# Kernel optimization log

Hardware: AMD Instinct MI355X
Metric: run time of the kernel (lower is better)

Reference implementation:

```python
import jax, jax.numpy as jnp
import numpy as np

C_IN = 64
C_INT = 32

def conv1x1(x, w, b):
    # x: [B,C,H,W], w: [O,C], b: [O]
    return jnp.einsum('bchw,oc->bohw', x, w) + b[None, :, None, None]

def maxpool2(x):
    # 2x2 max pool, stride 2. x: [B,C,H,W]
    B, C, H, W = x.shape
    return x.reshape(B, C, H // 2, 2, W // 2, 2).max(axis=(3, 5))

def setup_inputs() -> dict:
    key = jax.random.key(0)
    ks = jax.random.split(key, 9)
    s = 1.0 / np.sqrt(C_IN)
    si = 1.0 / np.sqrt(C_INT)
    x = jax.random.normal(ks[0], (16, C_IN, 64, 64), dtype=jnp.float32)
    return {
        'x': x,
        'w_origin': jax.random.normal(ks[1], (C_INT, C_IN), dtype=jnp.float32) * s,
        'b_origin': jax.random.normal(ks[2], (C_INT,), dtype=jnp.float32) * s,
        'w_theta': jax.random.normal(ks[3], (C_INT, C_IN), dtype=jnp.float32) * s,
        'b_theta': jax.random.normal(ks[4], (C_INT,), dtype=jnp.float32) * s,
        'w_phi': jax.random.normal(ks[5], (C_INT, C_IN), dtype=jnp.float32) * s,
        'b_phi': jax.random.normal(ks[6], (C_INT,), dtype=jnp.float32) * s,
        'w_W': jax.random.normal(ks[7], (C_IN, C_INT), dtype=jnp.float32) * si,
        'b_W': jax.random.normal(ks[8], (C_IN,), dtype=jnp.float32) * si,
    }

def reference(x, w_origin, b_origin, w_theta, b_theta, w_phi, b_phi, w_W, b_W):
    B, C, H, W = x.shape
    # value: conv1x1 + maxpool -> [B, Ci, H/2, W/2] -> [B, Nkv, Ci]
    f_x = maxpool2(conv1x1(x, w_origin, b_origin))
    f_x = f_x.reshape(B, C_INT, -1).transpose(0, 2, 1)
    # query: conv1x1 (no pooling) -> [B, N, Ci]
    theta_x = conv1x1(x, w_theta, b_theta).reshape(B, C_INT, -1).transpose(0, 2, 1)
    # key: conv1x1 + maxpool -> [B, Ci, Nkv]
    phi_x = maxpool2(conv1x1(x, w_phi, b_phi)).reshape(B, C_INT, -1)
    # attention: [B, N, Nkv]
    f = jnp.einsum('bnc,bcm->bnm', theta_x, phi_x)
    f_div_C = jax.nn.softmax(f, axis=-1)
    y = jnp.einsum('bnm,bmc->bnc', f_div_C, f_x)  # [B, N, Ci]
    y = y.transpose(0, 2, 1).reshape(B, C_INT, H, W)
    z = conv1x1(y, w_W, b_W) + x
    return z
```

## Files before the change

### kernel.cpp

```cpp
#include <hip/hip_runtime.h>
#include <math.h>


#define B_SZ 16
#define C_IN 64
#define C_INT 32
#define HW 4096
#define NKV 1024
#define PSTR 72
#define YSTR 40
#define CSTR 66
#define LOG2E 1.4426950408889634f

typedef __attribute__((ext_vector_type(8))) short bfrag;
typedef __attribute__((ext_vector_type(4))) float f32x4;

static __device__ __forceinline__ ushort f2bf(float v) {
  union { float f; uint u; } c; c.f = v;
  uint b = c.u + 0x7FFFu + ((c.u >> 16) & 1u);
  return (ushort)(b >> 16);
}
static __device__ __forceinline__ float bf2f(ushort h) {
  union { uint u; float f; } c; c.u = (uint)h << 16; return c.f;
}

__global__ __launch_bounds__(512) void k_qkv(
    const float* __restrict__ x,
    const float* __restrict__ wt, const float* __restrict__ bt,
    const float* __restrict__ wp, const float* __restrict__ bp,
    const float* __restrict__ wo, const float* __restrict__ bo,
    ushort* __restrict__ Qi, ushort* __restrict__ Ki, ushort* __restrict__ Vt) {
  __shared__ float sx[128 * CSTR];
  __shared__ float sPool[2][2][32][33];

  int t = threadIdx.x;
  int W = t >> 6, lane = t & 63, l15 = lane & 15, quad = lane >> 4;
  int bb = blockIdx.x >> 5, rg = blockIdx.x & 31;
  int p0 = rg * 128;

  #pragma unroll
  for (int i = 0; i < 4; ++i) {
    int f = i * 512 + t;
    int c = f >> 5, u = f & 31;
    float4 v = *(const float4*)(x + ((size_t)bb << 18) + (size_t)c * HW + p0 + 4 * u);
    sx[(4*u+0) * CSTR + c] = v.x;
    sx[(4*u+1) * CSTR + c] = v.y;
    sx[(4*u+2) * CSTR + c] = v.z;
    sx[(4*u+3) * CSTR + c] = v.w;
  }
  __syncthreads();

  int pix = W * 16 + l15;
  bfrag xh[2], xl[2];
  #pragma unroll
  for (int kh = 0; kh < 2; ++kh) {
    int base = pix * CSTR + kh * 32 + quad * 8;
    #pragma unroll
    for (int j2 = 0; j2 < 4; ++j2) {
      float2 d = *(const float2*)&sx[base + 2 * j2];
      ushort h0 = f2bf(d.x), h1 = f2bf(d.y);
      xh[kh][2*j2]   = (short)h0; xl[kh][2*j2]   = (short)f2bf(d.x - bf2f(h0));
      xh[kh][2*j2+1] = (short)h1; xl[kh][2*j2+1] = (short)f2bf(d.y - bf2f(h1));
    }
  }

  f32x4 acc[2];

  acc[0] = (f32x4){0.f,0.f,0.f,0.f}; acc[1] = (f32x4){0.f,0.f,0.f,0.f};
  #pragma unroll
  for (int kh = 0; kh < 2; ++kh)
    #pragma unroll
    for (int nt = 0; nt < 2; ++nt) {
      bfrag wh, wl;
      const float* wrow = wt + (size_t)(nt * 16 + l15) * 64 + kh * 32 + quad * 8;
      #pragma unroll
      for (int j = 0; j < 8; ++j) {
        float v = wrow[j] * LOG2E;
        ushort hb = f2bf(v);
        wh[j] = (short)hb; wl[j] = (short)f2bf(v - bf2f(hb));
      }
      acc[nt] = __builtin_amdgcn_mfma_f32_16x16x32_bf16(xh[kh], wh, acc[nt], 0, 0, 0);
      acc[nt] = __builtin_amdgcn_mfma_f32_16x16x32_bf16(xl[kh], wh, acc[nt], 0, 0, 0);
      acc[nt] = __builtin_amdgcn_mfma_f32_16x16x32_bf16(xh[kh], wl, acc[nt], 0, 0, 0);
    }
  #pragma unroll
  for (int nt = 0; nt < 2; ++nt) {
    float bias = bt[nt * 16 + l15] * LOG2E;
    ushort* qb = Qi + ((size_t)bb * HW + p0 + W * 16) * 64 + nt * 16 + l15;
    #pragma unroll
    for (int r = 0; r < 4; ++r) {
      float v = acc[nt][r] + bias;
      ushort hb = f2bf(v);
      qb[(size_t)(quad * 4 + r) * 64]      = hb;
      qb[(size_t)(quad * 4 + r) * 64 + 32] = f2bf(v - bf2f(hb));
    }
  }

  int prow = (W * 16 + quad * 4) >> 6;
  int px2  = ((W * 16 + quad * 4) & 63) >> 1;

  acc[0] = (f32x4){0.f,0.f,0.f,0.f}; acc[1] = (f32x4){0.f,0.f,0.f,0.f};
  #pragma unroll
  for (int kh = 0; kh < 2; ++kh)
    #pragma unroll
    for (int nt = 0; nt < 2; ++nt) {
      bfrag wh, wl;
      const float* wrow = wp + (size_t)(nt * 16 + l15) * 64 + kh * 32 + quad * 8;
      #pragma unroll
      for (int j = 0; j < 8; ++j) {
        float v = wrow[j];
        ushort hb = f2bf(v);
        wh[j] = (short)hb; wl[j] = (short)f2bf(v - bf2f(hb));
      }
      acc[nt] = __builtin_amdgcn_mfma_f32_16x16x32_bf16(xh[kh], wh, acc[nt], 0, 0, 0);
      acc[nt] = __builtin_amdgcn_mfma_f32_16x16x32_bf16(xl[kh], wh, acc[nt], 0, 0, 0);
      acc[nt] = __builtin_amdgcn_mfma_f32_16x16x32_bf16(xh[kh], wl, acc[nt], 0, 0, 0);
    }
  #pragma unroll
  for (int nt = 0; nt < 2; ++nt) {
    float bias = bp[nt * 16 + l15];
    sPool[0][prow][px2    ][nt * 16 + l15] = fmaxf(acc[nt][0], acc[nt][1]) + bias;
    sPool[0][prow][px2 + 1][nt * 16 + l15] = fmaxf(acc[nt][2], acc[nt][3]) + bias;
  }

  acc[0] = (f32x4){0.f,0.f,0.f,0.f}; acc[1] = (f32x4){0.f,0.f,0.f,0.f};
  #pragma unroll
  for (int kh = 0; kh < 2; ++kh)
    #pragma unroll
    for (int nt = 0; nt < 2; ++nt) {
      bfrag wh;
      const float* wrow = wo + (size_t)(nt * 16 + l15) * 64 + kh * 32 + quad * 8;
      #pragma unroll
      for (int j = 0; j < 8; ++j) wh[j] = (short)f2bf(wrow[j]);
      acc[nt] = __builtin_amdgcn_mfma_f32_16x16x32_bf16(xh[kh], wh, acc[nt], 0, 0, 0);
      acc[nt] = __builtin_amdgcn_mfma_f32_16x16x32_bf16(xl[kh], wh, acc[nt], 0, 0, 0);
    }
  #pragma unroll
  for (int nt = 0; nt < 2; ++nt) {
    float bias = bo[nt * 16 + l15];
    sPool[1][prow][px2    ][nt * 16 + l15] = fmaxf(acc[nt][0], acc[nt][1]) + bias;
    sPool[1][prow][px2 + 1][nt * 16 + l15] = fmaxf(acc[nt][2], acc[nt][3]) + bias;
  }
  __syncthreads();

  for (int f = t; f < 1024; f += 512) {
    int px = f >> 5, ch = f & 31;
    float v = fmaxf(sPool[0][0][px][ch], sPool[0][1][px][ch]);
    ushort hb = f2bf(v);
    size_t idx = ((size_t)bb * NKV + rg * 32 + px) * 64 + ch;
    Ki[idx] = hb;
    Ki[idx + 32] = f2bf(v - bf2f(hb));
  }
  for (int f = t; f < 1024; f += 512) {
    int ch = f >> 5, px = f & 31;
    float v = fmaxf(sPool[1][0][px][ch], sPool[1][1][px][ch]);
    Vt[(size_t)bb * 32 * NKV + (size_t)ch * NKV + rg * 32 + px] = f2bf(v);
  }
}

__global__ __launch_bounds__(256, 3) void k_attn(
    const ushort* __restrict__ Qi, const ushort* __restrict__ Ki,
    const ushort* __restrict__ Vt,
    const float* __restrict__ x, const float* __restrict__ wW,
    const float* __restrict__ bW, float* __restrict__ z) {
  __shared__ __align__(16) ushort sP[4 * 64 * PSTR];
  __shared__ __align__(16) ushort sY[2 * 64 * YSTR];

  int t = threadIdx.x;
  int w = t >> 6, lane = t & 63, l15 = lane & 15, quad = lane >> 4;
  int bb = blockIdx.x >> 6;
  int p0 = (blockIdx.x & 63) << 6;

  const ushort* Qb = Qi + ((size_t)bb * HW + p0) * 64;
  const ushort* Kb = Ki + ((size_t)bb * NKV + (size_t)w * 256) * 64;
  const ushort* Vb = Vt + (size_t)bb * 32 * NKV + (size_t)w * 256;
  ushort* myP = sP + w * 64 * PSTR;

  bfrag qh[4], ql[4];
  #pragma unroll
  for (int mt = 0; mt < 4; ++mt) {
    const ushort* qp = Qb + (size_t)(mt * 16 + l15) * 64 + quad * 8;
    qh[mt] = *(const bfrag*)qp;
    ql[mt] = *(const bfrag*)(qp + 32);
  }

  bfrag kh[4], kl[4], vb[2][2];
  auto loadK = [&](int sc) {
    #pragma unroll
    for (int tt = 0; tt < 4; ++tt) {
      const ushort* p = Kb + (size_t)(sc * 64 + tt * 16 + l15) * 64 + quad * 8;
      kh[tt] = *(const bfrag*)p;
      kl[tt] = *(const bfrag*)(p + 32);
    }
  };
  auto loadV = [&](int sc) {
    #pragma unroll
    for (int ks = 0; ks < 2; ++ks)
      #pragma unroll
      for (int nt = 0; nt < 2; ++nt)
        vb[ks][nt] = *(const bfrag*)(Vb + (size_t)(nt * 16 + l15) * NKV
                                        + sc * 64 + ks * 32 + quad * 8);
  };

  f32x4 accO[4][2], accS[4];
  #pragma unroll
  for (int mt = 0; mt < 4; ++mt) {
    accS[mt] = (f32x4){0.f,0.f,0.f,0.f};
    accO[mt][0] = (f32x4){0.f,0.f,0.f,0.f};
    accO[mt][1] = (f32x4){0.f,0.f,0.f,0.f};
  }
  bfrag vones;
  #pragma unroll
  for (int i = 0; i < 8; ++i) vones[i] = (short)0x3F80;

  loadK(0);
  for (int sc = 0; sc < 4; ++sc) {
    loadV(sc);
    #pragma unroll
    for (int tt = 0; tt < 4; ++tt)
      #pragma unroll
      for (int mt = 0; mt < 4; ++mt) {
        f32x4 s = (f32x4){0.f,0.f,0.f,0.f};
        s = __builtin_amdgcn_mfma_f32_16x16x32_bf16(kh[tt], qh[mt], s, 0, 0, 0);
        s = __builtin_amdgcn_mfma_f32_16x16x32_bf16(kh[tt], ql[mt], s, 0, 0, 0);
        s = __builtin_amdgcn_mfma_f32_16x16x32_bf16(kl[tt], qh[mt], s, 0, 0, 0);
        float e0 = exp2f(s[0]), e1 = exp2f(s[1]);
        float e2 = exp2f(s[2]), e3 = exp2f(s[3]);
        uint2 pk;
        pk.x = (__float_as_uint(e0) >> 16) | (__float_as_uint(e1) & 0xFFFF0000u);
        pk.y = (__float_as_uint(e2) >> 16) | (__float_as_uint(e3) & 0xFFFF0000u);
        *(uint2*)&myP[(mt * 16 + l15) * PSTR + tt * 16 + quad * 4] = pk;
      }
    if (sc < 3) loadK(sc + 1);
    #pragma unroll
    for (int ks = 0; ks < 2; ++ks)
      #pragma unroll
      for (int mt = 0; mt < 4; ++mt) {
        bfrag a = *(const bfrag*)&myP[(mt * 16 + l15) * PSTR + ks * 32 + quad * 8];
        accO[mt][0] = __builtin_amdgcn_mfma_f32_16x16x32_bf16(a, vb[ks][0], accO[mt][0], 0, 0, 0);
        accO[mt][1] = __builtin_amdgcn_mfma_f32_16x16x32_bf16(a, vb[ks][1], accO[mt][1], 0, 0, 0);
        accS[mt]    = __builtin_amdgcn_mfma_f32_16x16x32_bf16(a, vones,     accS[mt],    0, 0, 0);
      }
  }

  __syncthreads();
  float* mrg = (float*)sP;
  float* sS  = mrg + 4 * 64 * 33;
  #pragma unroll
  for (int mt = 0; mt < 4; ++mt)
    #pragma unroll
    for (int r = 0; r < 4; ++r) {
      int q = mt * 16 + quad * 4 + r;
      mrg[(w * 64 + q) * 33 + l15]      = accO[mt][0][r];
      mrg[(w * 64 + q) * 33 + 16 + l15] = accO[mt][1][r];
      if (l15 == 0) sS[w * 64 + q] = accS[mt][r];
    }
  __syncthreads();

  #pragma unroll
  for (int i = 0; i < 8; ++i) {
    int e = i * 256 + t;
    int q = e >> 5, ch = e & 31;
    float v = mrg[q * 33 + ch] + mrg[(64 + q) * 33 + ch]
            + mrg[(128 + q) * 33 + ch] + mrg[(192 + q) * 33 + ch];
    float ssum = sS[q] + sS[64 + q] + sS[128 + q] + sS[192 + q];
    float y = v * __builtin_amdgcn_rcpf(ssum);
    ushort hb = f2bf(y);
    sY[q * YSTR + ch] = hb;
    sY[64 * YSTR + q * YSTR + ch] = f2bf(y - bf2f(hb));
  }
  __syncthreads();

  bfrag ah, al;
  {
    const float* wrow = wW + (size_t)(w * 16 + l15) * 32 + quad * 8;
    #pragma unroll
    for (int j = 0; j < 8; ++j) {
      float v = wrow[j];
      ushort hb = f2bf(v);
      ah[j] = (short)hb; al[j] = (short)f2bf(v - bf2f(hb));
    }
  }
  float bWr[4];
  #pragma unroll
  for (int r = 0; r < 4; ++r) bWr[r] = bW[w * 16 + quad * 4 + r];
  #pragma unroll
  for (int nt = 0; nt < 4; ++nt) {
    bfrag yh = *(const bfrag*)&sY[(nt * 16 + l15) * YSTR + quad * 8];
    bfrag yl = *(const bfrag*)&sY[64 * YSTR + (nt * 16 + l15) * YSTR + quad * 8];
    f32x4 d = (f32x4){0.f,0.f,0.f,0.f};
    d = __builtin_amdgcn_mfma_f32_16x16x32_bf16(ah, yh, d, 0, 0, 0);
    d = __builtin_amdgcn_mfma_f32_16x16x32_bf16(al, yh, d, 0, 0, 0);
    d = __builtin_amdgcn_mfma_f32_16x16x32_bf16(ah, yl, d, 0, 0, 0);
    #pragma unroll
    for (int r = 0; r < 4; ++r) {
      size_t zi = ((size_t)bb << 18) + ((size_t)(w * 16 + quad * 4 + r) << 12)
                + p0 + nt * 16 + l15;
      z[zi] = d[r] + bWr[r] + x[zi];
    }
  }
}

extern "C" void kernel_launch(void* const* d_in, const int* in_sizes, int n_in,
                              void* d_out, int out_size, void* d_ws, size_t ws_size,
                              hipStream_t stream) {
  const float* x   = (const float*)d_in[0];
  const float* w_o = (const float*)d_in[1];
  const float* b_o = (const float*)d_in[2];
  const float* w_t = (const float*)d_in[3];
  const float* b_t = (const float*)d_in[4];
  const float* w_p = (const float*)d_in[5];
  const float* b_p = (const float*)d_in[6];
  const float* w_W = (const float*)d_in[7];
  const float* b_W = (const float*)d_in[8];
  float* z = (float*)d_out;

  ushort* Qi = (ushort*)d_ws;
  ushort* Ki = Qi + (size_t)B_SZ * HW * 64;
  ushort* Vt = Ki + (size_t)B_SZ * NKV * 64;

  k_qkv<<<dim3(B_SZ * 32), dim3(512), 0, stream>>>(
      x, w_t, b_t, w_p, b_p, w_o, b_o, Qi, Ki, Vt);
  k_attn<<<dim3(B_SZ * 64), dim3(256), 0, stream>>>(
      Qi, Ki, Vt, x, w_W, b_W, z);
}
```

Measured before the change: 131.3 us.

## Store Q/K/V in MFMA fragment order and keep P in registers

The projection kernel now writes Q, K and V as split hi/lo bf16 arrays pre-permuted into MFMA fragment order, so the attention kernel loads each fragment with one contiguous vector load. The attention loop computes S transposed (K as the A operand), which lets the exp'd probabilities feed the 16x16x16 MFMA directly from registers, removing the shared-memory round trip for P. Row sums are accumulated with VALU adds plus shuffles instead of a ones-vector MFMA, and K/V tiles are double-buffered. Launch bounds are raised to 4 blocks per SM. The cost is more complex index math in the producer kernel and scattered 2-byte stores for K and V.

Result: faster. 128.0 us (-2.5%).

```diff
diff --git a/kernel.cpp b/kernel.cpp
--- a/kernel.cpp
+++ b/kernel.cpp
@@ -3,16 +3,14 @@
 
 
 #define B_SZ 16
-#define C_IN 64
-#define C_INT 32
 #define HW 4096
 #define NKV 1024
-#define PSTR 72
-#define YSTR 40
-#define CSTR 66
+#define XSTR 65
+#define YS 40
 #define LOG2E 1.4426950408889634f
 
 typedef __attribute__((ext_vector_type(8))) short bfrag;
+typedef __attribute__((ext_vector_type(4))) short sfrag;
 typedef __attribute__((ext_vector_type(4))) float f32x4;
 
 static __device__ __forceinline__ ushort f2bf(float v) {
@@ -29,8 +27,9 @@
     const float* __restrict__ wt, const float* __restrict__ bt,
     const float* __restrict__ wp, const float* __restrict__ bp,
     const float* __restrict__ wo, const float* __restrict__ bo,
-    ushort* __restrict__ Qi, ushort* __restrict__ Ki, ushort* __restrict__ Vt) {
-  __shared__ float sx[128 * CSTR];
+    ushort* __restrict__ QH, ushort* __restrict__ QL,
+    ushort* __restrict__ KH, ushort* __restrict__ KL, ushort* __restrict__ VF) {
+  __shared__ float sx[128 * XSTR];
   __shared__ float sPool[2][2][32][33];
 
   int t = threadIdx.x;
@@ -43,57 +42,51 @@
     int f = i * 512 + t;
     int c = f >> 5, u = f & 31;
     float4 v = *(const float4*)(x + ((size_t)bb << 18) + (size_t)c * HW + p0 + 4 * u);
-    sx[(4*u+0) * CSTR + c] = v.x;
-    sx[(4*u+1) * CSTR + c] = v.y;
-    sx[(4*u+2) * CSTR + c] = v.z;
-    sx[(4*u+3) * CSTR + c] = v.w;
+    sx[(4*u+0) * XSTR + c] = v.x;
+    sx[(4*u+1) * XSTR + c] = v.y;
+    sx[(4*u+2) * XSTR + c] = v.z;
+    sx[(4*u+3) * XSTR + c] = v.w;
   }
   __syncthreads();
 
   int pix = W * 16 + l15;
   bfrag xh[2], xl[2];
   #pragma unroll
-  for (int kh = 0; kh < 2; ++kh) {
-    int base = pix * CSTR + kh * 32 + quad * 8;
-    #pragma unroll
-    for (int j2 = 0; j2 < 4; ++j2) {
-      float2 d = *(const float2*)&sx[base + 2 * j2];
-      ushort h0 = f2bf(d.x), h1 = f2bf(d.y);
-      xh[kh][2*j2]   = (short)h0; xl[kh][2*j2]   = (short)f2bf(d.x - bf2f(h0));
-      xh[kh][2*j2+1] = (short)h1; xl[kh][2*j2+1] = (short)f2bf(d.y - bf2f(h1));
-    }
-  }
+  for (int kh2 = 0; kh2 < 2; ++kh2)
+    #pragma unroll
+    for (int j = 0; j < 8; ++j) {
+      float v = sx[pix * XSTR + kh2 * 32 + quad * 8 + j];
+      ushort hb = f2bf(v);
+      xh[kh2][j] = (short)hb;
+      xl[kh2][j] = (short)f2bf(v - bf2f(hb));
+    }
+  __syncthreads();
 
   f32x4 acc[2];
 
   acc[0] = (f32x4){0.f,0.f,0.f,0.f}; acc[1] = (f32x4){0.f,0.f,0.f,0.f};
   #pragma unroll
-  for (int kh = 0; kh < 2; ++kh)
+  for (int kh2 = 0; kh2 < 2; ++kh2)
     #pragma unroll
     for (int nt = 0; nt < 2; ++nt) {
       bfrag wh, wl;
-      const float* wrow = wt + (size_t)(nt * 16 + l15) * 64 + kh * 32 + quad * 8;
+      const float* wrow = wt + (size_t)(nt * 16 + l15) * 64 + kh2 * 32 + quad * 8;
       #pragma unroll
       for (int j = 0; j < 8; ++j) {
         float v = wrow[j] * LOG2E;
         ushort hb = f2bf(v);
         wh[j] = (short)hb; wl[j] = (short)f2bf(v - bf2f(hb));
       }
-      acc[nt] = __builtin_amdgcn_mfma_f32_16x16x32_bf16(xh[kh], wh, acc[nt], 0, 0, 0);
-      acc[nt] = __builtin_amdgcn_mfma_f32_16x16x32_bf16(xl[kh], wh, acc[nt], 0, 0, 0);
-      acc[nt] = __builtin_amdgcn_mfma_f32_16x16x32_bf16(xh[kh], wl, acc[nt], 0, 0, 0);
+      acc[nt] = __builtin_amdgcn_mfma_f32_16x16x32_bf16(xh[kh2], wh, acc[nt], 0, 0, 0);
+      acc[nt] = __builtin_amdgcn_mfma_f32_16x16x32_bf16(xl[kh2], wh, acc[nt], 0, 0, 0);
+      acc[nt] = __builtin_amdgcn_mfma_f32_16x16x32_bf16(xh[kh2], wl, acc[nt], 0, 0, 0);
     }
   #pragma unroll
   for (int nt = 0; nt < 2; ++nt) {
     float bias = bt[nt * 16 + l15] * LOG2E;
-    ushort* qb = Qi + ((size_t)bb * HW + p0 + W * 16) * 64 + nt * 16 + l15;
-    #pragma unroll
-    for (int r = 0; r < 4; ++r) {
-      float v = acc[nt][r] + bias;
-      ushort hb = f2bf(v);
-      qb[(size_t)(quad * 4 + r) * 64]      = hb;
-      qb[(size_t)(quad * 4 + r) * 64 + 32] = f2bf(v - bf2f(hb));
-    }
+    #pragma unroll
+    for (int r = 0; r < 4; ++r)
+      sx[(W * 16 + quad * 4 + r) * XSTR + nt * 16 + l15] = acc[nt][r] + bias;
   }
 
   int prow = (W * 16 + quad * 4) >> 6;
@@ -101,20 +94,20 @@
 
   acc[0] = (f32x4){0.f,0.f,0.f,0.f}; acc[1] = (f32x4){0.f,0.f,0.f,0.f};
   #pragma unroll
-  for (int kh = 0; kh < 2; ++kh)
+  for (int kh2 = 0; kh2 < 2; ++kh2)
     #pragma unroll
     for (int nt = 0; nt < 2; ++nt) {
       bfrag wh, wl;
-      const float* wrow = wp + (size_t)(nt * 16 + l15) * 64 + kh * 32 + quad * 8;
+      const float* wrow = wp + (size_t)(nt * 16 + l15) * 64 + kh2 * 32 + quad * 8;
       #pragma unroll
       for (int j = 0; j < 8; ++j) {
         float v = wrow[j];
         ushort hb = f2bf(v);
         wh[j] = (short)hb; wl[j] = (short)f2bf(v - bf2f(hb));
       }
-      acc[nt] = __builtin_amdgcn_mfma_f32_16x16x32_bf16(xh[kh], wh, acc[nt], 0, 0, 0);
-      acc[nt] = __builtin_amdgcn_mfma_f32_16x16x32_bf16(xl[kh], wh, acc[nt], 0, 0, 0);
-      acc[nt] = __builtin_amdgcn_mfma_f32_16x16x32_bf16(xh[kh], wl, acc[nt], 0, 0, 0);
+      acc[nt] = __builtin_amdgcn_mfma_f32_16x16x32_bf16(xh[kh2], wh, acc[nt], 0, 0, 0);
+      acc[nt] = __builtin_amdgcn_mfma_f32_16x16x32_bf16(xl[kh2], wh, acc[nt], 0, 0, 0);
+      acc[nt] = __builtin_amdgcn_mfma_f32_16x16x32_bf16(xh[kh2], wl, acc[nt], 0, 0, 0);
     }
   #pragma unroll
   for (int nt = 0; nt < 2; ++nt) {
@@ -125,15 +118,15 @@
 
   acc[0] = (f32x4){0.f,0.f,0.f,0.f}; acc[1] = (f32x4){0.f,0.f,0.f,0.f};
   #pragma unroll
-  for (int kh = 0; kh < 2; ++kh)
+  for (int kh2 = 0; kh2 < 2; ++kh2)
     #pragma unroll
     for (int nt = 0; nt < 2; ++nt) {
       bfrag wh;
-      const float* wrow = wo + (size_t)(nt * 16 + l15) * 64 + kh * 32 + quad * 8;
+      const float* wrow = wo + (size_t)(nt * 16 + l15) * 64 + kh2 * 32 + quad * 8;
       #pragma unroll
       for (int j = 0; j < 8; ++j) wh[j] = (short)f2bf(wrow[j]);
-      acc[nt] = __builtin_amdgcn_mfma_f32_16x16x32_bf16(xh[kh], wh, acc[nt], 0, 0, 0);
-      acc[nt] = __builtin_amdgcn_mfma_f32_16x16x32_bf16(xl[kh], wh, acc[nt], 0, 0, 0);
+      acc[nt] = __builtin_amdgcn_mfma_f32_16x16x32_bf16(xh[kh2], wh, acc[nt], 0, 0, 0);
+      acc[nt] = __builtin_amdgcn_mfma_f32_16x16x32_bf16(xl[kh2], wh, acc[nt], 0, 0, 0);
     }
   #pragma unroll
   for (int nt = 0; nt < 2; ++nt) {
@@ -143,160 +136,188 @@
   }
   __syncthreads();
 
+  {
+    int qt = t >> 6, ln = t & 63, fl = ln & 15, fq = ln >> 4;
+    union { ushort u[8]; uint4 v; } Hh, Ll;
+    #pragma unroll
+    for (int j = 0; j < 8; ++j) {
+      float v = sx[(qt * 16 + fl) * XSTR + fq * 8 + j];
+      ushort hb = f2bf(v);
+      Hh.u[j] = hb;
+      Ll.u[j] = f2bf(v - bf2f(hb));
+    }
+    size_t base = ((size_t)(bb * 256 + rg * 8 + qt) * 64 + ln) * 8;
+    *(uint4*)(QH + base) = Hh.v;
+    *(uint4*)(QL + base) = Ll.v;
+  }
+
+  #pragma unroll
   for (int f = t; f < 1024; f += 512) {
-    int px = f >> 5, ch = f & 31;
-    float v = fmaxf(sPool[0][0][px][ch], sPool[0][1][px][ch]);
+    int tt = f >> 9, rem = f & 511;
+    int ln = rem >> 3, j = rem & 7;
+    int kvl = tt * 16 + (ln & 15);
+    int ch = (ln >> 4) * 8 + j;
+    float v = fmaxf(sPool[0][0][kvl][ch], sPool[0][1][kvl][ch]);
     ushort hb = f2bf(v);
-    size_t idx = ((size_t)bb * NKV + rg * 32 + px) * 64 + ch;
-    Ki[idx] = hb;
-    Ki[idx + 32] = f2bf(v - bf2f(hb));
-  }
+    size_t base = ((size_t)(bb * 64 + rg * 2 + tt) * 64 + ln) * 8 + j;
+    KH[base] = hb;
+    KL[base] = f2bf(v - bf2f(hb));
+  }
+
+  #pragma unroll
   for (int f = t; f < 1024; f += 512) {
-    int ch = f >> 5, px = f & 31;
-    float v = fmaxf(sPool[1][0][px][ch], sPool[1][1][px][ch]);
-    Vt[(size_t)bb * 32 * NKV + (size_t)ch * NKV + rg * 32 + px] = f2bf(v);
-  }
-}
-
-__global__ __launch_bounds__(256, 3) void k_attn(
-    const ushort* __restrict__ Qi, const ushort* __restrict__ Ki,
-    const ushort* __restrict__ Vt,
+    int tt = f >> 9, mt = (f >> 8) & 1;
+    int ln = (f >> 2) & 63, j = f & 3;
+    int kvl = tt * 16 + ((ln >> 4) << 2) + j;
+    int ch = mt * 16 + (ln & 15);
+    float v = fmaxf(sPool[1][0][kvl][ch], sPool[1][1][kvl][ch]);
+    VF[(((size_t)(bb * 64 + rg * 2 + tt) * 2 + mt) * 64 + ln) * 4 + j] = f2bf(v);
+  }
+}
+
+__global__ __launch_bounds__(256, 4) void k_attn(
+    const ushort* __restrict__ QH, const ushort* __restrict__ QL,
+    const ushort* __restrict__ KH, const ushort* __restrict__ KL,
+    const ushort* __restrict__ VF,
     const float* __restrict__ x, const float* __restrict__ wW,
     const float* __restrict__ bW, float* __restrict__ z) {
-  __shared__ __align__(16) ushort sP[4 * 64 * PSTR];
-  __shared__ __align__(16) ushort sY[2 * 64 * YSTR];
+  __shared__ float smem[4 * 64 * 36 + 4 * 64];
+  float* mrg = smem;
+  float* sS  = smem + 4 * 64 * 36;
 
   int t = threadIdx.x;
   int w = t >> 6, lane = t & 63, l15 = lane & 15, quad = lane >> 4;
   int bb = blockIdx.x >> 6;
-  int p0 = (blockIdx.x & 63) << 6;
-
-  const ushort* Qb = Qi + ((size_t)bb * HW + p0) * 64;
-  const ushort* Kb = Ki + ((size_t)bb * NKV + (size_t)w * 256) * 64;
-  const ushort* Vb = Vt + (size_t)bb * 32 * NKV + (size_t)w * 256;
-  ushort* myP = sP + w * 64 * PSTR;
+  int bq = blockIdx.x & 63;
 
   bfrag qh[4], ql[4];
   #pragma unroll
-  for (int mt = 0; mt < 4; ++mt) {
-    const ushort* qp = Qb + (size_t)(mt * 16 + l15) * 64 + quad * 8;
-    qh[mt] = *(const bfrag*)qp;
-    ql[mt] = *(const bfrag*)(qp + 32);
-  }
-
-  bfrag kh[4], kl[4], vb[2][2];
-  auto loadK = [&](int sc) {
-    #pragma unroll
-    for (int tt = 0; tt < 4; ++tt) {
-      const ushort* p = Kb + (size_t)(sc * 64 + tt * 16 + l15) * 64 + quad * 8;
-      kh[tt] = *(const bfrag*)p;
-      kl[tt] = *(const bfrag*)(p + 32);
-    }
+  for (int qt = 0; qt < 4; ++qt) {
+    size_t base = ((size_t)(bb * 256 + bq * 4 + qt) * 64 + lane) * 8;
+    qh[qt] = *(const bfrag*)(QH + base);
+    ql[qt] = *(const bfrag*)(QL + base);
+  }
+
+  const ushort* KHb = KH + (size_t)bb * 64 * 64 * 8;
+  const ushort* KLb = KL + (size_t)bb * 64 * 64 * 8;
+  const ushort* VFb = VF + (size_t)bb * 64 * 2 * 64 * 4;
+
+  f32x4 accO[4][2];
+  float spart[4] = {0.f, 0.f, 0.f, 0.f};
+  #pragma unroll
+  for (int qt = 0; qt < 4; ++qt) {
+    accO[qt][0] = (f32x4){0.f,0.f,0.f,0.f};
+    accO[qt][1] = (f32x4){0.f,0.f,0.f,0.f};
+  }
+
+  bfrag kh[2], kl[2];
+  sfrag vf[2][2];
+  auto loadT = [&](int buf, int i) {
+    int gt = w * 16 + i;
+    size_t kb = ((size_t)gt * 64 + lane) * 8;
+    kh[buf] = *(const bfrag*)(KHb + kb);
+    kl[buf] = *(const bfrag*)(KLb + kb);
+    vf[buf][0] = *(const sfrag*)(VFb + (((size_t)gt * 2 + 0) * 64 + lane) * 4);
+    vf[buf][1] = *(const sfrag*)(VFb + (((size_t)gt * 2 + 1) * 64 + lane) * 4);
   };
-  auto loadV = [&](int sc) {
-    #pragma unroll
-    for (int ks = 0; ks < 2; ++ks)
+
+  loadT(0, 0);
+  #pragma unroll 2
+  for (int i = 0; i < 16; ++i) {
+    int cur = i & 1;
+    if (i < 15) loadT(cur ^ 1, i + 1);
+    #pragma unroll
+    for (int qt = 0; qt < 4; ++qt) {
+      f32x4 s = (f32x4){0.f,0.f,0.f,0.f};
+      s = __builtin_amdgcn_mfma_f32_16x16x32_bf16(kh[cur], qh[qt], s, 0, 0, 0);
+      s = __builtin_amdgcn_mfma_f32_16x16x32_bf16(kh[cur], ql[qt], s, 0, 0, 0);
+      s = __builtin_amdgcn_mfma_f32_16x16x32_bf16(kl[cur], qh[qt], s, 0, 0, 0);
+      float e0 = exp2f(s[0]), e1 = exp2f(s[1]);
+      float e2 = exp2f(s[2]), e3 = exp2f(s[3]);
+      spart[qt] += (e0 + e1) + (e2 + e3);
+      union { uint2 u; sfrag s4; } pk;
+      pk.u.x = (__float_as_uint(e0) >> 16) | (__float_as_uint(e1) & 0xFFFF0000u);
+      pk.u.y = (__float_as_uint(e2) >> 16) | (__float_as_uint(e3) & 0xFFFF0000u);
+      accO[qt][0] = __builtin_amdgcn_mfma_f32_16x16x16bf16_1k(vf[cur][0], pk.s4, accO[qt][0], 0, 0, 0);
+      accO[qt][1] = __builtin_amdgcn_mfma_f32_16x16x16bf16_1k(vf[cur][1], pk.s4, accO[qt][1], 0, 0, 0);
+    }
+  }
+
+  #pragma unroll
+  for (int qt = 0; qt < 4; ++qt) {
+    spart[qt] += __shfl_xor(spart[qt], 16);
+    spart[qt] += __shfl_xor(spart[qt], 32);
+  }
+
+  #pragma unroll
+  for (int qt = 0; qt < 4; ++qt) {
+    #pragma unroll
+    for (int mt = 0; mt < 2; ++mt)
+      *(float4*)&mrg[((size_t)w * 64 + qt * 16 + l15) * 36 + mt * 16 + quad * 4] =
+          make_float4(accO[qt][mt][0], accO[qt][mt][1], accO[qt][mt][2], accO[qt][mt][3]);
+    if (lane < 16) sS[w * 64 + qt * 16 + l15] = spart[qt];
+  }
+  __syncthreads();
+
+  int rq = t >> 2, rc = (t & 3) * 8;
+  float yv[8];
+  {
+    float ssum = sS[rq] + sS[64 + rq] + sS[128 + rq] + sS[192 + rq];
+    float inv = 1.0f / ssum;
+    #pragma unroll
+    for (int h = 0; h < 2; ++h) {
+      float4 a = *(const float4*)&mrg[(size_t)rq * 36 + rc + 4 * h];
+      float4 b = *(const float4*)&mrg[(size_t)(64 + rq) * 36 + rc + 4 * h];
+      float4 c = *(const float4*)&mrg[(size_t)(128 + rq) * 36 + rc + 4 * h];
+      float4 d = *(const float4*)&mrg[(size_t)(192 + rq) * 36 + rc + 4 * h];
+      yv[4*h+0] = (a.x + b.x + c.x + d.x) * inv;
+      yv[4*h+1] = (a.y + b.y + c.y + d.y) * inv;
+      yv[4*h+2] = (a.z + b.z + c.z + d.z) * inv;
+      yv[4*h+3] = (a.w + b.w + c.w + d.w) * inv;
+    }
+  }
+  __syncthreads();
+
+  ushort* yH = (ushort*)mrg;
+  ushort* yL = yH + 64 * YS;
+  {
+    union { ushort u[8]; uint4 v; } Hh, Ll;
+    #pragma unroll
+    for (int j = 0; j < 8; ++j) {
+      ushort hb = f2bf(yv[j]);
+      Hh.u[j] = hb;
+      Ll.u[j] = f2bf(yv[j] - bf2f(hb));
+    }
+    *(uint4*)&yH[rq * YS + rc] = Hh.v;
+    *(uint4*)&yL[rq * YS + rc] = Ll.v;
+  }
+  __syncthreads();
+
+  #pragma unroll
+  for (int nt = 0; nt < 4; ++nt) {
+    f32x4 d = (f32x4){0.f,0.f,0.f,0.f};
+    #pragma unroll
+    for (int kt = 0; kt < 2; ++kt) {
+      float4 w4 = *(const float4*)&wW[(size_t)(w * 16 + l15) * 32 + kt * 16 + quad * 4];
+      sfrag ah, al, yhf, ylf;
       #pragma unroll
-      for (int nt = 0; nt < 2; ++nt)
-        vb[ks][nt] = *(const bfrag*)(Vb + (size_t)(nt * 16 + l15) * NKV
-                                        + sc * 64 + ks * 32 + quad * 8);
-  };
-
-  f32x4 accO[4][2], accS[4];
-  #pragma unroll
-  for (int mt = 0; mt < 4; ++mt) {
-    accS[mt] = (f32x4){0.f,0.f,0.f,0.f};
-    accO[mt][0] = (f32x4){0.f,0.f,0.f,0.f};
-    accO[mt][1] = (f32x4){0.f,0.f,0.f,0.f};
-  }
-  bfrag vones;
-  #pragma unroll
-  for (int i = 0; i < 8; ++i) vones[i] = (short)0x3F80;
-
-  loadK(0);
-  for (int sc = 0; sc < 4; ++sc) {
-    loadV(sc);
-    #pragma unroll
-    for (int tt = 0; tt < 4; ++tt)
-      #pragma unroll
-      for (int mt = 0; mt < 4; ++mt) {
-        f32x4 s = (f32x4){0.f,0.f,0.f,0.f};
-        s = __builtin_amdgcn_mfma_f32_16x16x32_bf16(kh[tt], qh[mt], s, 0, 0, 0);
-        s = __builtin_amdgcn_mfma_f32_16x16x32_bf16(kh[tt], ql[mt], s, 0, 0, 0);
-        s = __builtin_amdgcn_mfma_f32_16x16x32_bf16(kl[tt], qh[mt], s, 0, 0, 0);
-        float e0 = exp2f(s[0]), e1 = exp2f(s[1]);
-        float e2 = exp2f(s[2]), e3 = exp2f(s[3]);
-        uint2 pk;
-        pk.x = (__float_as_uint(e0) >> 16) | (__float_as_uint(e1) & 0xFFFF0000u);
-        pk.y = (__float_as_uint(e2) >> 16) | (__float_as_uint(e3) & 0xFFFF0000u);
-        *(uint2*)&myP[(mt * 16 + l15) * PSTR + tt * 16 + quad * 4] = pk;
+      for (int j = 0; j < 4; ++j) {
+        float v = (&w4.x)[j];
+        ushort hb = f2bf(v);
+        ah[j] = (short)hb; al[j] = (short)f2bf(v - bf2f(hb));
       }
-    if (sc < 3) loadK(sc + 1);
-    #pragma unroll
-    for (int ks = 0; ks < 2; ++ks)
-      #pragma unroll
-      for (int mt = 0; mt < 4; ++mt) {
-        bfrag a = *(const bfrag*)&myP[(mt * 16 + l15) * PSTR + ks * 32 + quad * 8];
-        accO[mt][0] = __builtin_amdgcn_mfma_f32_16x16x32_bf16(a, vb[ks][0], accO[mt][0], 0, 0, 0);
-        accO[mt][1] = __builtin_amdgcn_mfma_f32_16x16x32_bf16(a, vb[ks][1], accO[mt][1], 0, 0, 0);
-        accS[mt]    = __builtin_amdgcn_mfma_f32_16x16x32_bf16(a, vones,     accS[mt],    0, 0, 0);
-      }
-  }
-
-  __syncthreads();
-  float* mrg = (float*)sP;
-  float* sS  = mrg + 4 * 64 * 33;
-  #pragma unroll
-  for (int mt = 0; mt < 4; ++mt)
+      yhf = *(const sfrag*)&yH[(nt * 16 + l15) * YS + kt * 16 + quad * 4];
+      ylf = *(const sfrag*)&yL[(nt * 16 + l15) * YS + kt * 16 + quad * 4];
+      d = __builtin_amdgcn_mfma_f32_16x16x16bf16_1k(ah, yhf, d, 0, 0, 0);
+      d = __builtin_amdgcn_mfma_f32_16x16x16bf16_1k(al, yhf, d, 0, 0, 0);
+      d = __builtin_amdgcn_mfma_f32_16x16x16bf16_1k(ah, ylf, d, 0, 0, 0);
+    }
     #pragma unroll
     for (int r = 0; r < 4; ++r) {
-      int q = mt * 16 + quad * 4 + r;
-      mrg[(w * 64 + q) * 33 + l15]      = accO[mt][0][r];
-      mrg[(w * 64 + q) * 33 + 16 + l15] = accO[mt][1][r];
-      if (l15 == 0) sS[w * 64 + q] = accS[mt][r];
-    }
-  __syncthreads();
-
-  #pragma unroll
-  for (int i = 0; i < 8; ++i) {
-    int e = i * 256 + t;
-    int q = e >> 5, ch = e & 31;
-    float v = mrg[q * 33 + ch] + mrg[(64 + q) * 33 + ch]
-            + mrg[(128 + q) * 33 + ch] + mrg[(192 + q) * 33 + ch];
-    float ssum = sS[q] + sS[64 + q] + sS[128 + q] + sS[192 + q];
-    float y = v * __builtin_amdgcn_rcpf(ssum);
-    ushort hb = f2bf(y);
-    sY[q * YSTR + ch] = hb;
-    sY[64 * YSTR + q * YSTR + ch] = f2bf(y - bf2f(hb));
-  }
-  __syncthreads();
-
-  bfrag ah, al;
-  {
-    const float* wrow = wW + (size_t)(w * 16 + l15) * 32 + quad * 8;
-    #pragma unroll
-    for (int j = 0; j < 8; ++j) {
-      float v = wrow[j];
-      ushort hb = f2bf(v);
-      ah[j] = (short)hb; al[j] = (short)f2bf(v - bf2f(hb));
-    }
-  }
-  float bWr[4];
-  #pragma unroll
-  for (int r = 0; r < 4; ++r) bWr[r] = bW[w * 16 + quad * 4 + r];
-  #pragma unroll
-  for (int nt = 0; nt < 4; ++nt) {
-    bfrag yh = *(const bfrag*)&sY[(nt * 16 + l15) * YSTR + quad * 8];
-    bfrag yl = *(const bfrag*)&sY[64 * YSTR + (nt * 16 + l15) * YSTR + quad * 8];
-    f32x4 d = (f32x4){0.f,0.f,0.f,0.f};
-    d = __builtin_amdgcn_mfma_f32_16x16x32_bf16(ah, yh, d, 0, 0, 0);
-    d = __builtin_amdgcn_mfma_f32_16x16x32_bf16(al, yh, d, 0, 0, 0);
-    d = __builtin_amdgcn_mfma_f32_16x16x32_bf16(ah, yl, d, 0, 0, 0);
-    #pragma unroll
-    for (int r = 0; r < 4; ++r) {
-      size_t zi = ((size_t)bb << 18) + ((size_t)(w * 16 + quad * 4 + r) << 12)
-                + p0 + nt * 16 + l15;
-      z[zi] = d[r] + bWr[r] + x[zi];
+      int cout = w * 16 + quad * 4 + r;
+      size_t zi = ((size_t)bb << 18) + ((size_t)cout << 12)
+                + (size_t)(bq * 4 + nt) * 16 + l15;
+      z[zi] = d[r] + bW[cout] + x[zi];
     }
   }
 }
@@ -315,12 +336,14 @@
   const float* b_W = (const float*)d_in[8];
   float* z = (float*)d_out;
 
-  ushort* Qi = (ushort*)d_ws;
-  ushort* Ki = Qi + (size_t)B_SZ * HW * 64;
-  ushort* Vt = Ki + (size_t)B_SZ * NKV * 64;
+  ushort* QH = (ushort*)d_ws;
+  ushort* QL = QH + 2097152;
+  ushort* KH = QL + 2097152;
+  ushort* KL = KH + 524288;
+  ushort* VF = KL + 524288;
 
   k_qkv<<<dim3(B_SZ * 32), dim3(512), 0, stream>>>(
-      x, w_t, b_t, w_p, b_p, w_o, b_o, Qi, Ki, Vt);
+      x, w_t, b_t, w_p, b_p, w_o, b_o, QH, QL, KH, KL, VF);
   k_attn<<<dim3(B_SZ * 64), dim3(256), 0, stream>>>(
-      Qi, Ki, Vt, x, w_W, b_W, z);
-}
+      QH, QL, KH, KL, VF, x, w_W, b_W, z);
+}
```
